# Kernel optimization log

Hardware: AMD Instinct MI355X
Metric: run time of the kernel (lower is better)

The kernel has to match this reference:

```python
import jax, jax.numpy as jnp
import numpy as np

B, S, D = 2, 2048, 2048
H, KVH, HD = 16, 4, 128
R = 128
WINDOW, GLOBAL = 512, 64
THETA = 1000000.0


def setup_inputs() -> dict:
    key = jax.random.key(0)
    ks = jax.random.split(key, 13)
    def rn(k, shape, s=0.02):
        return jax.random.normal(k, shape, dtype=jnp.float32) * s
    return {
        'x': jax.random.normal(ks[0], (B, S, D), dtype=jnp.float32),
        'wq_w': rn(ks[1], (H * HD, D)), 'wq_a': rn(ks[2], (R, D)), 'wq_b': rn(ks[3], (H * HD, R)),
        'wk_w': rn(ks[4], (KVH * HD, D)), 'wk_a': rn(ks[5], (R, D)), 'wk_b': rn(ks[6], (KVH * HD, R)),
        'wv_w': rn(ks[7], (KVH * HD, D)), 'wv_a': rn(ks[8], (R, D)), 'wv_b': rn(ks[9], (KVH * HD, R)),
        'wo_w': rn(ks[10], (D, H * HD)), 'wo_a': rn(ks[11], (R, H * HD)), 'wo_b': rn(ks[12], (D, R)),
    }


def _lora_linear(x, w, a, b):
    # F.linear(x, w) + F.linear(F.linear(x, A), B)
    return x @ w.T + (x @ a.T) @ b.T


def _apply_rope(x, cos, sin):
    # view_as_complex pairs consecutive elements: (x0,x1),(x2,x3),...
    xr, xi = x[..., 0::2], x[..., 1::2]
    out_r = xr * cos - xi * sin
    out_i = xr * sin + xi * cos
    return jnp.stack([out_r, out_i], axis=-1).reshape(x.shape)


def reference(x, wq_w, wq_a, wq_b, wk_w, wk_a, wk_b, wv_w, wv_a, wv_b, wo_w, wo_a, wo_b):
    # RoPE frequencies (scaling_factor=1.0 -> plain RoPE; YaRN ramp is identity)
    inv_freq = 1.0 / (THETA ** (jnp.arange(0, HD, 2, dtype=jnp.float32) / HD))
    t = jnp.arange(S, dtype=jnp.float32)
    freqs = t[:, None] * inv_freq[None, :]           # [S, HD/2]
    cos = jnp.cos(freqs)[None, :, None, :]           # [1,S,1,HD/2]
    sin = jnp.sin(freqs)[None, :, None, :]

    q = _lora_linear(x, wq_w, wq_a, wq_b).reshape(B, S, H, HD)
    k = _lora_linear(x, wk_w, wk_a, wk_b).reshape(B, S, KVH, HD)
    v = _lora_linear(x, wv_w, wv_a, wv_b).reshape(B, S, KVH, HD)

    q = _apply_rope(q, cos, sin)
    k = _apply_rope(k, cos, sin)

    # GQA: repeat kv heads
    g = H // KVH
    k = jnp.repeat(k, g, axis=2)
    v = jnp.repeat(v, g, axis=2)

    scores = jnp.einsum('bqhd,bkhd->bhqk', q, k) / jnp.sqrt(jnp.float32(HD))
    i = jnp.arange(S)[:, None]
    j = jnp.arange(S)[None, :]
    # causal + local sliding window + global tokens (attended by all)
    allowed = (j <= i) & (((i - j) < WINDOW) | (j < GLOBAL))
    scores = jnp.where(allowed[None, None], scores, jnp.float32(-1e9))
    p = jax.nn.softmax(scores, axis=-1)
    out = jnp.einsum('bhqk,bkhd->bqhd', p, v).reshape(B, S, H * HD)
    return _lora_linear(out, wo_w, wo_a, wo_b)
```

## Files before the change

kernel.cpp:

```cpp
#include <hip/hip_runtime.h>

#define B_ 2
#define S_LEN 2048
#define DMODEL 2048
#define NH 16
#define NKVH 4
#define HD 128
#define RLORA 128
#define WINDOW_ 512
#define NGLOBAL 64

#define FENCE asm volatile("" ::: "memory")

typedef __bf16 bf16x8 __attribute__((ext_vector_type(8)));
typedef float f32x4 __attribute__((ext_vector_type(4)));

__device__ __forceinline__ float bf2f(unsigned short h) {
    return __uint_as_float(((unsigned int)h) << 16);
}
__device__ __forceinline__ unsigned short f2bf(float f) {
    unsigned int u = __float_as_uint(f);
    unsigned int r = u + 0x7fffu + ((u >> 16) & 1u);
    return (unsigned short)(r >> 16);
}
__device__ __forceinline__ unsigned int pack2bf(float a, float b) {
    return (unsigned int)f2bf(a) | ((unsigned int)f2bf(b) << 16);
}
__device__ __forceinline__ uint4 load8f(const float* p) {
    float4 f0 = *(const float4*)p;
    float4 f1 = *(const float4*)(p + 4);
    uint4 u;
    u.x = pack2bf(f0.x, f0.y);
    u.y = pack2bf(f0.z, f0.w);
    u.z = pack2bf(f1.x, f1.y);
    u.w = pack2bf(f1.z, f1.w);
    return u;
}

__device__ __forceinline__ void gld16(const unsigned short* g, unsigned short* l) {
    __builtin_amdgcn_global_load_lds(
        (const __attribute__((address_space(1))) unsigned int*)g,
        (__attribute__((address_space(3))) unsigned int*)l,
        16, 0, 0);
}

struct Conv12 {
    const float* s[12];
    unsigned short* d[12];
    int c[13];
};
__global__ __launch_bounds__(256) void convk(Conv12 a)
{
    int b = blockIdx.x;
    int seg = 0;
    while (b >= a.c[seg + 1]) seg++;
    int off = (b - a.c[seg]) * 2048 + threadIdx.x * 8;
    *(uint4*)(a.d[seg] + off) = load8f(a.s[seg] + off);
}

struct TransA4 { const float* s[4]; unsigned short* d[4]; };
__global__ __launch_bounds__(256) void transAk(TransA4 a)
{
    __shared__ float tile[32][65];
    const int bid = blockIdx.x;
    const int mat = bid >> 7;
    const int tl = bid & 127;
    const int rt = tl & 3, ct = tl >> 2;
    const float* src = a.s[mat];
    unsigned short* dst = a.d[mat];
    const int t = threadIdx.x;
    #pragma unroll
    for (int p = 0; p < 2; p++) {
        int r = p * 16 + (t >> 4);
        int c = (t & 15) * 4;
        float4 v = *(const float4*)(src + (size_t)(rt * 32 + r) * 2048 + ct * 64 + c);
        tile[r][c] = v.x; tile[r][c + 1] = v.y;
        tile[r][c + 2] = v.z; tile[r][c + 3] = v.w;
    }
    __syncthreads();
    const int n = t >> 2, r8 = (t & 3) * 8;
    uint4 u;
    u.x = pack2bf(tile[r8 + 0][n], tile[r8 + 1][n]);
    u.y = pack2bf(tile[r8 + 2][n], tile[r8 + 3][n]);
    u.z = pack2bf(tile[r8 + 4][n], tile[r8 + 5][n]);
    u.w = pack2bf(tile[r8 + 6][n], tile[r8 + 7][n]);
    *(uint4*)(dst + (size_t)(ct * 64 + n) * 128 + rt * 32 + r8) = u;
}

__global__ __launch_bounds__(256) void weffk(
    unsigned short* __restrict__ C, int ldc,
    const unsigned short* __restrict__ Bm,
    const unsigned short* __restrict__ At,
    int seg)
{
    const int m0 = blockIdx.x * 128;
    const int n0 = blockIdx.y * 128;
    const unsigned short* Atb = At;
    if (seg)
        Atb = At + ((m0 < 2048) ? 0 : (m0 < 2560) ? (2048 * 128) : (2 * 2048 * 128));
    __shared__ __align__(16) unsigned short As_[128 * 32];
    __shared__ __align__(16) unsigned short Bs_[128 * 32];
    const int tid = threadIdx.x, lane = tid & 63, wid = tid >> 6;
    const int quad = lane >> 4, l16 = lane & 15;
    const int lr = lane >> 2, lc8 = (lane & 3) * 8;
    const int wm0 = (wid >> 1) * 64, wn0 = (wid & 1) * 64;
    f32x4 acc[4][4] = {};
    for (int k0 = 0; k0 < 128; k0 += 32) {
        #pragma unroll
        for (int c = 0; c < 2; c++) {
            int chunk = wid * 2 + c;
            gld16(Bm + (size_t)(m0 + chunk * 16 + lr) * 128 + k0 + lc8, As_ + chunk * 512);
            gld16(Atb + (size_t)(n0 + chunk * 16 + lr) * 128 + k0 + lc8, Bs_ + chunk * 512);
        }
        __syncthreads();
        bf16x8 af[4], bf[4];
        #pragma unroll
        for (int i = 0; i < 4; i++)
            af[i] = *(const bf16x8*)&As_[(wm0 + i * 16 + l16) * 32 + quad * 8];
        #pragma unroll
        for (int j = 0; j < 4; j++)
            bf[j] = *(const bf16x8*)&Bs_[(wn0 + j * 16 + l16) * 32 + quad * 8];
        #pragma unroll
        for (int i = 0; i < 4; i++)
            #pragma unroll
            for (int j = 0; j < 4; j++)
                acc[i][j] = __builtin_amdgcn_mfma_f32_16x16x32_bf16(af[i], bf[j], acc[i][j], 0, 0, 0);
        __syncthreads();
    }
    #pragma unroll
    for (int i = 0; i < 4; i++)
        #pragma unroll
        for (int j = 0; j < 4; j++) {
            const int col = n0 + wn0 + j * 16 + l16;
            #pragma unroll
            for (int r = 0; r < 4; r++) {
                size_t idx = (size_t)(m0 + wm0 + i * 16 + quad * 4 + r) * ldc + col;
                C[idx] = f2bf(bf2f(C[idx]) + acc[i][j][r]);
            }
        }
}

__device__ __forceinline__ void gemm128_acc(
    const unsigned short* __restrict__ A, int lda, int m0,
    const unsigned short* __restrict__ W, int ldw, int n0,
    int Kmain, f32x4 (&acc)[4][4])
{
    __shared__ __align__(16) unsigned short As[2][4096];
    __shared__ __align__(16) unsigned short Bs[2][4096];
    const int tid = threadIdx.x;
    const int lane = tid & 63, wid = tid >> 6;
    const int quad = lane >> 4, l16 = lane & 15;
    const int wm = (wid >> 1) * 64, wn = (wid & 1) * 64;

    int arow[2], acol[2];
    #pragma unroll
    for (int c = 0; c < 2; c++) {
        const int o = tid * 16 + c * 4096;
        arow[c] = o >> 6;
        acol[c] = (((tid & 3) * 16) ^ (((arow[c] >> 1) & 3) << 4)) >> 1;
    }

    const int nt = Kmain >> 5;

    auto stage = [&](int bb, int j) {
        const int k0 = j << 5;
        #pragma unroll
        for (int c = 0; c < 2; c++)
            gld16(A + (size_t)(m0 + arow[c]) * lda + k0 + acol[c],
                  &As[bb][tid * 8 + c * 2048]);
        #pragma unroll
        for (int c = 0; c < 2; c++)
            gld16(W + (size_t)(n0 + arow[c]) * ldw + k0 + acol[c],
                  &Bs[bb][tid * 8 + c * 2048]);
    };

    const int xoff = (((quad * 16) ^ (((l16 >> 1) & 3) << 4)) >> 1);
    const int ard = (wm + l16) * 32 + xoff;
    const int brd = (wn + l16) * 32 + xoff;

    stage(0, 0);
    stage(1, 1);

    for (int t = 0; t < nt; t++) {
        const int bb = t & 1;
        if (t < nt - 1) {
            asm volatile("s_waitcnt vmcnt(4)" ::: "memory");
        } else {
            asm volatile("s_waitcnt vmcnt(0)" ::: "memory");
        }
        __builtin_amdgcn_sched_barrier(0);
        FENCE; __builtin_amdgcn_s_barrier(); FENCE;

        bf16x8 af[4], bfn[4];
        #pragma unroll
        for (int mi = 0; mi < 4; mi++)
            af[mi] = *(const bf16x8*)&As[bb][ard + mi * 512];
        #pragma unroll
        for (int ni = 0; ni < 4; ni++)
            bfn[ni] = *(const bf16x8*)&Bs[bb][brd + ni * 512];

        __builtin_amdgcn_s_setprio(1);
        #pragma unroll
        for (int mi = 0; mi < 4; mi++)
            #pragma unroll
            for (int ni = 0; ni < 4; ni++)
                acc[mi][ni] = __builtin_amdgcn_mfma_f32_16x16x32_bf16(
                    af[mi], bfn[ni], acc[mi][ni], 0, 0, 0);
        __builtin_amdgcn_s_setprio(0);

        FENCE; __builtin_amdgcn_s_barrier(); FENCE;
        if (t + 2 < nt) stage(bb, t + 2);
    }
}

__device__ __forceinline__ f32x4 rope4(f32x4 v, int col, int rowbase)
{
    const int t2 = col & 127;
    const float invf = __expf(-(float)(t2 >> 1) * (13.815510557964274f / 64.0f));
    const bool ev = (t2 & 1) == 0;
    f32x4 o;
    #pragma unroll
    for (int r = 0; r < 4; r++) {
        float self = v[r];
        float other = __shfl_xor(self, 1);
        float pos = (float)((rowbase + r) & (S_LEN - 1));
        float s, c;
        __sincosf(pos * invf, &s, &c);
        o[r] = ev ? (self * c - other * s) : (other * s + self * c);
    }
    return o;
}

__global__ __launch_bounds__(256, 3) void gemm128_qkv(
    const unsigned short* __restrict__ Xb,
    const unsigned short* __restrict__ Wqkv,
    unsigned short* __restrict__ Qo, unsigned short* __restrict__ Ko,
    unsigned short* __restrict__ Vt)
{
    const int m0 = blockIdx.x * 128;
    const int n0 = blockIdx.y * 128;
    f32x4 acc[4][4] = {};
    gemm128_acc(Xb, DMODEL, m0, Wqkv, DMODEL, n0, DMODEL, acc);

    const int tid = threadIdx.x, lane = tid & 63, wid = tid >> 6;
    const int l16 = lane & 15, quad = lane >> 4;
    const int wm = (wid >> 1) * 64, wn = (wid & 1) * 64;

    if (n0 < 2048) {
        #pragma unroll
        for (int mi = 0; mi < 4; mi++)
            #pragma unroll
            for (int ni = 0; ni < 4; ni++) {
                const int col = n0 + wn + ni * 16 + l16;
                const int rb = m0 + wm + mi * 16 + quad * 4;
                f32x4 v = rope4(acc[mi][ni], col, rb);
                #pragma unroll
                for (int r = 0; r < 4; r++)
                    Qo[(size_t)(rb + r) * DMODEL + col] = f2bf(v[r]);
            }
    } else if (n0 < 2560) {
        #pragma unroll
        for (int mi = 0; mi < 4; mi++)
            #pragma unroll
            for (int ni = 0; ni < 4; ni++) {
                const int col = n0 - 2048 + wn + ni * 16 + l16;
                const int rb = m0 + wm + mi * 16 + quad * 4;
                f32x4 v = rope4(acc[mi][ni], col, rb);
                #pragma unroll
                for (int r = 0; r < 4; r++)
                    Ko[(size_t)(rb + r) * 512 + col] = f2bf(v[r]);
            }
    } else {
        const int b = m0 >> 11;
        #pragma unroll
        for (int mi = 0; mi < 4; mi++)
            #pragma unroll
            for (int ni = 0; ni < 4; ni++) {
                const int ncol = n0 - 2560 + wn + ni * 16 + l16;
                const int head = ncol >> 7, dd = ncol & 127;
                const int srow = (m0 & (S_LEN - 1)) + wm + mi * 16 + quad * 4;
                uint2 pk;
                pk.x = pack2bf(acc[mi][ni][0], acc[mi][ni][1]);
                pk.y = pack2bf(acc[mi][ni][2], acc[mi][ni][3]);
                *(uint2*)(Vt + ((size_t)(b * NKVH + head) * HD + dd) * S_LEN + srow) = pk;
            }
    }
}

__global__ __launch_bounds__(256, 3) void gemm128_out(
    const unsigned short* __restrict__ Xb,
    const unsigned short* __restrict__ Ww,
    float* __restrict__ Out)
{
    const int m0 = blockIdx.x * 128;
    const int n0 = blockIdx.y * 128;
    f32x4 acc[4][4] = {};
    gemm128_acc(Xb, DMODEL, m0, Ww, DMODEL, n0, DMODEL, acc);

    const int tid = threadIdx.x, lane = tid & 63, wid = tid >> 6;
    const int l16 = lane & 15, quad = lane >> 4;
    const int wm = (wid >> 1) * 64, wn = (wid & 1) * 64;
    #pragma unroll
    for (int mi = 0; mi < 4; mi++)
        #pragma unroll
        for (int ni = 0; ni < 4; ni++) {
            const int col = n0 + wn + ni * 16 + l16;
            const size_t rb = (size_t)(m0 + wm + mi * 16 + quad * 4);
            #pragma unroll
            for (int r = 0; r < 4; r++)
                Out[(rb + r) * DMODEL + col] = acc[mi][ni][r];
        }
}

__global__ __launch_bounds__(256, 2) void attn_mfma(
    const unsigned short* __restrict__ Q,
    const unsigned short* __restrict__ K,
    const unsigned short* __restrict__ Vt,
    unsigned short* __restrict__ O)
{
    __shared__ __align__(16) unsigned short kvbuf[2][8192];
    __shared__ unsigned short plds[4][32 * 40];
    const int tid = threadIdx.x, lane = tid & 63, wid = tid >> 6;
    const int l16 = lane & 15, quad = lane >> 4;
    const int bid = blockIdx.x;
    const int g   = bid & 7;
    const int kvh = g & 3;
    const int b   = g >> 2;
    const int qt  = 63 - (bid >> 3);
    const int q0  = qt * 32;
    const int h   = kvh * 4 + wid;

    const unsigned short* qrow0 = Q + ((size_t)(b * S_LEN + q0 + l16)) * DMODEL + h * HD;
    bf16x8 qf0[4], qf1[4];
    #pragma unroll
    for (int c = 0; c < 4; c++) {
        qf0[c] = *(const bf16x8*)(qrow0 + c * 32 + quad * 8);
        qf1[c] = *(const bf16x8*)(qrow0 + (size_t)16 * DMODEL + c * 32 + quad * 8);
    }

    const unsigned short* Kbase  = K + ((size_t)(b * S_LEN)) * (NKVH * HD) + kvh * HD;
    const unsigned short* Vplane = Vt + ((size_t)(b * NKVH + kvh) * HD) * S_LEN;
    unsigned short* pw = &plds[wid][0];

    const unsigned short* Ksrc[2];
    const unsigned short* Vsrc[2];
    #pragma unroll
    for (int c = 0; c < 2; c++) {
        const int o = wid * 2048 + c * 1024 + lane * 16;
        const int kkey = o >> 8;
        const int kdim = (o & 255) ^ ((kkey & 15) << 4);
        Ksrc[c] = Kbase + (size_t)kkey * (NKVH * HD) + (kdim >> 1);
        const int vd = o >> 6;
        const int vkb = (o & 63) ^ ((vd & 3) << 4);
        Vsrc[c] = Vplane + (size_t)vd * S_LEN + (vkb >> 1);
    }

    f32x4 oacc0[8] = {}, oacc1[8] = {};
    f32x4 lrow0 = {0.f, 0.f, 0.f, 0.f}, lrow1 = {0.f, 0.f, 0.f, 0.f};
    const float c2 = 0.12753102f;

    const int kthi = (q0 + 31) >> 5;
    int wlo = q0 - (WINDOW_ - 1); if (wlo < 0) wlo = 0;
    const int ktw = wlo >> 5;

    auto nexttile = [&](int t) -> int {
        if (t < ktw) { int u = t + 1; return (u < 2 && u < ktw) ? u : ktw; }
        return t + 1;
    };

    auto stage = [&](int buf, int ktb) {
        #pragma unroll
        for (int c = 0; c < 2; c++) {
            gld16(Ksrc[c] + (size_t)ktb * (NKVH * HD),
                  &kvbuf[buf][wid * 1024 + c * 512]);
            gld16(Vsrc[c] + ktb,
                  &kvbuf[buf][4096 + wid * 1024 + c * 512]);
        }
    };

    int kt = 0;
    stage(0, 0);
    __syncthreads();
    int cur = 0;

    while (true) {
        const int ktb = kt * 32;
        const int ktn = nexttile(kt);
        const bool last = (ktn > kthi);
        if (!last) stage(cur ^ 1, ktn * 32);

        const unsigned short* kb  = kvbuf[cur];
        const unsigned short* vbp = kvbuf[cur] + 4096;

        bf16x8 kf0[4], kf1[4];
        #pragma unroll
        for (int c = 0; c < 4; c++) {
            const int koff = (l16 * 256 + ((c * 64 + quad * 16) ^ (l16 << 4))) >> 1;
            kf0[c] = *(const bf16x8*)&kb[koff];
            kf1[c] = *(const bf16x8*)&kb[koff + 2048];
        }

        f32x4 s00 = {}, s01 = {}, s10 = {}, s11 = {};
        __builtin_amdgcn_s_setprio(1);
        #pragma unroll
        for (int c = 0; c < 4; c++) {
            s00 = __builtin_amdgcn_mfma_f32_16x16x32_bf16(qf0[c], kf0[c], s00, 0, 0, 0);
            s01 = __builtin_amdgcn_mfma_f32_16x16x32_bf16(qf0[c], kf1[c], s01, 0, 0, 0);
            s10 = __builtin_amdgcn_mfma_f32_16x16x32_bf16(qf1[c], kf0[c], s10, 0, 0, 0);
            s11 = __builtin_amdgcn_mfma_f32_16x16x32_bf16(qf1[c], kf1[c], s11, 0, 0, 0);
        }
        __builtin_amdgcn_s_setprio(0);

        #pragma unroll
        for (int s = 0; s < 2; s++) {
            const f32x4 sa0 = s ? s10 : s00;
            const f32x4 sa1 = s ? s11 : s01;
            const int qs = q0 + s * 16;
            const bool full = (ktb + 31 <= qs) &&
                              (((qs + 15) - ktb < WINDOW_) || (ktb + 31 < NGLOBAL));
            f32x4& lr = s ? lrow1 : lrow0;
            #pragma unroll
            for (int rr = 0; rr < 4; rr++) {
                float p0 = exp2f(sa0[rr] * c2);
                float p1 = exp2f(sa1[rr] * c2);
                if (!full) {
                    const int i = qs + quad * 4 + rr;
                    const int j0 = ktb + l16, j1 = j0 + 16;
                    bool a0 = (j0 <= i) && ((i - j0 < WINDOW_) || (j0 < NGLOBAL));
                    bool a1 = (j1 <= i) && ((i - j1 < WINDOW_) || (j1 < NGLOBAL));
                    p0 = a0 ? p0 : 0.f;
                    p1 = a1 ? p1 : 0.f;
                }
                lr[rr] += p0 + p1;
                pw[(s * 16 + quad * 4 + rr) * 40 + l16]      = f2bf(p0);
                pw[(s * 16 + quad * 4 + rr) * 40 + 16 + l16] = f2bf(p1);
            }
        }
        bf16x8 pa0 = *(const bf16x8*)(pw + l16 * 40 + quad * 8);
        bf16x8 pa1 = *(const bf16x8*)(pw + (16 + l16) * 40 + quad * 8);

        {
            bf16x8 va[4];
            #pragma unroll
            for (int ds = 0; ds < 4; ds++) {
                const int d = ds * 16 + l16;
                va[ds] = *(const bf16x8*)&vbp[(d * 64 + ((quad * 16) ^ ((l16 & 3) << 4))) >> 1];
            }
            __builtin_amdgcn_s_setprio(1);
            #pragma unroll
            for (int ds = 0; ds < 4; ds++) {
                oacc0[ds] = __builtin_amdgcn_mfma_f32_16x16x32_bf16(pa0, va[ds], oacc0[ds], 0, 0, 0);
                oacc1[ds] = __builtin_amdgcn_mfma_f32_16x16x32_bf16(pa1, va[ds], oacc1[ds], 0, 0, 0);
            }
            __builtin_amdgcn_s_setprio(0);
        }
        {
            bf16x8 vb[4];
            #pragma unroll
            for (int ds = 0; ds < 4; ds++) {
                const int d = (ds + 4) * 16 + l16;
                vb[ds] = *(const bf16x8*)&vbp[(d * 64 + ((quad * 16) ^ ((l16 & 3) << 4))) >> 1];
            }
            __builtin_amdgcn_s_setprio(1);
            #pragma unroll
            for (int ds = 0; ds < 4; ds++) {
                oacc0[ds + 4] = __builtin_amdgcn_mfma_f32_16x16x32_bf16(pa0, vb[ds], oacc0[ds + 4], 0, 0, 0);
                oacc1[ds + 4] = __builtin_amdgcn_mfma_f32_16x16x32_bf16(pa1, vb[ds], oacc1[ds + 4], 0, 0, 0);
            }
            __builtin_amdgcn_s_setprio(0);
        }

        if (last) break;
        __syncthreads();
        cur ^= 1;
        kt = ktn;
    }

    #pragma unroll
    for (int off = 1; off <= 8; off <<= 1) {
        #pragma unroll
        for (int rr = 0; rr < 4; rr++) {
            lrow0[rr] += __shfl_xor(lrow0[rr], off);
            lrow1[rr] += __shfl_xor(lrow1[rr], off);
        }
    }

    #pragma unroll
    for (int s = 0; s < 2; s++) {
        const f32x4& lr = s ? lrow1 : lrow0;
        #pragma unroll
        for (int rr = 0; rr < 4; rr++) {
            float inv = 1.f / lr[rr];
            unsigned short* orow = O + ((size_t)(b * S_LEN + q0 + s * 16 + quad * 4 + rr)) * DMODEL + h * HD;
            #pragma unroll
            for (int ds = 0; ds < 8; ds++) {
                float v = s ? oacc1[ds][rr] : oacc0[ds][rr];
                orow[ds * 16 + l16] = f2bf(v * inv);
            }
        }
    }
}

extern "C" void kernel_launch(void* const* d_in, const int* in_sizes, int n_in,
                              void* d_out, int out_size, void* d_ws, size_t ws_size,
                              hipStream_t stream)
{
    const float* x    = (const float*)d_in[0];
    const float* wq_w = (const float*)d_in[1];
    const float* wq_a = (const float*)d_in[2];
    const float* wq_b = (const float*)d_in[3];
    const float* wk_w = (const float*)d_in[4];
    const float* wk_a = (const float*)d_in[5];
    const float* wk_b = (const float*)d_in[6];
    const float* wv_w = (const float*)d_in[7];
    const float* wv_a = (const float*)d_in[8];
    const float* wv_b = (const float*)d_in[9];
    const float* wo_w = (const float*)d_in[10];
    const float* wo_a = (const float*)d_in[11];
    const float* wo_b = (const float*)d_in[12];

    char* ws = (char*)d_ws;
    unsigned short* wqkvb  = (unsigned short*)(ws);
    unsigned short* apackT = (unsigned short*)(ws + 12582912);
    unsigned short* bqkvb  = (unsigned short*)(ws + 14155776);
    unsigned short* Qbuf   = (unsigned short*)(ws + 18087936);
    unsigned short* Kbuf   = (unsigned short*)(ws + 34865152);
    unsigned short* Vtbuf  = (unsigned short*)(ws + 39059456);
    unsigned short* wowb   = (unsigned short*)(ws);
    unsigned short* wobb   = (unsigned short*)(ws + 8388608);
    unsigned short* woabT  = (unsigned short*)(ws + 8912896);
    unsigned short* xb = (unsigned short*)d_out;

    Conv12 c1;
    c1.s[0] = x;    c1.d[0] = xb;
    c1.s[1] = wq_w; c1.d[1] = wqkvb;
    c1.s[2] = wk_w; c1.d[2] = wqkvb + 2048 * 2048;
    c1.s[3] = wv_w; c1.d[3] = wqkvb + 2560 * 2048;
    c1.s[4] = wq_b; c1.d[4] = bqkvb;
    c1.s[5] = wk_b; c1.d[5] = bqkvb + 2048 * 128;
    c1.s[6] = wv_b; c1.d[6] = bqkvb + 2560 * 128;
    for (int i = 7; i < 12; i++) { c1.s[i] = wv_b; c1.d[i] = bqkvb + 2560 * 128; }
    int cum1[13] = {0, 4096, 6144, 6656, 7168, 7296, 7328, 7360, 7360, 7360,
                    7360, 7360, 7360};
    for (int i = 0; i < 13; i++) c1.c[i] = cum1[i];
    convk<<<dim3(7360), dim3(256), 0, stream>>>(c1);

    TransA4 t1;
    t1.s[0] = wq_a; t1.d[0] = apackT;
    t1.s[1] = wk_a; t1.d[1] = apackT + 2048 * 128;
    t1.s[2] = wv_a; t1.d[2] = apackT + 2 * 2048 * 128;
    t1.s[3] = wq_a; t1.d[3] = apackT;
    transAk<<<dim3(384), dim3(256), 0, stream>>>(t1);

    weffk<<<dim3(24, 16), dim3(256), 0, stream>>>(wqkvb, DMODEL, bqkvb, apackT, 1);

    gemm128_qkv<<<dim3(32, 24), dim3(256), 0, stream>>>(
        xb, wqkvb, Qbuf, Kbuf, Vtbuf);

    Conv12 c2;
    c2.s[0] = wo_w; c2.d[0] = wowb;
    c2.s[1] = wo_b; c2.d[1] = wobb;
    for (int i = 2; i < 12; i++) { c2.s[i] = wo_b; c2.d[i] = wobb; }
    int cum2[13] = {0, 2048, 2176, 2176, 2176, 2176, 2176, 2176, 2176, 2176,
                    2176, 2176, 2176};
    for (int i = 0; i < 13; i++) c2.c[i] = cum2[i];
    convk<<<dim3(2176), dim3(256), 0, stream>>>(c2);

    TransA4 t2;
    t2.s[0] = wo_a; t2.d[0] = woabT;
    t2.s[1] = wo_a; t2.d[1] = woabT;
    t2.s[2] = wo_a; t2.d[2] = woabT;
    t2.s[3] = wo_a; t2.d[3] = woabT;
    transAk<<<dim3(128), dim3(256), 0, stream>>>(t2);

    weffk<<<dim3(16, 16), dim3(256), 0, stream>>>(wowb, DMODEL, wobb, woabT, 0);

    attn_mfma<<<dim3(512), dim3(256), 0, stream>>>(Qbuf, Kbuf, Vtbuf, Qbuf);

    gemm128_out<<<dim3(32, 16), dim3(256), 0, stream>>>(
        Qbuf, wowb, (float*)d_out);
}
```

Before: 317.0 us.

## Fuse weight fp32 conversion into LoRA merge, triple-buffer GEMM, raise attention occupancy

```diff
diff --git a/kernel.cpp b/kernel.cpp
--- a/kernel.cpp
+++ b/kernel.cpp
@@ -89,6 +89,8 @@
 
 __global__ __launch_bounds__(256) void weffk(
     unsigned short* __restrict__ C, int ldc,
+    const float* __restrict__ W0, const float* __restrict__ W1,
+    const float* __restrict__ W2,
     const unsigned short* __restrict__ Bm,
     const unsigned short* __restrict__ At,
     int seg)
@@ -96,8 +98,12 @@
     const int m0 = blockIdx.x * 128;
     const int n0 = blockIdx.y * 128;
     const unsigned short* Atb = At;
-    if (seg)
-        Atb = At + ((m0 < 2048) ? 0 : (m0 < 2560) ? (2048 * 128) : (2 * 2048 * 128));
+    const float* Wsrc = W0;
+    int wrow = m0;
+    if (seg) {
+        if (m0 >= 2560)      { Atb = At + 2 * 2048 * 128; Wsrc = W2; wrow = m0 - 2560; }
+        else if (m0 >= 2048) { Atb = At + 2048 * 128;     Wsrc = W1; wrow = m0 - 2048; }
+    }
     __shared__ __align__(16) unsigned short As_[128 * 32];
     __shared__ __align__(16) unsigned short Bs_[128 * 32];
     const int tid = threadIdx.x, lane = tid & 63, wid = tid >> 6;
@@ -134,8 +140,9 @@
             const int col = n0 + wn0 + j * 16 + l16;
             #pragma unroll
             for (int r = 0; r < 4; r++) {
-                size_t idx = (size_t)(m0 + wm0 + i * 16 + quad * 4 + r) * ldc + col;
-                C[idx] = f2bf(bf2f(C[idx]) + acc[i][j][r]);
+                const int row = wm0 + i * 16 + quad * 4 + r;
+                float w = Wsrc[(size_t)(wrow + row) * 2048 + col];
+                C[(size_t)(m0 + row) * ldc + col] = f2bf(w + acc[i][j][r]);
             }
         }
 }
@@ -145,8 +152,8 @@
     const unsigned short* __restrict__ W, int ldw, int n0,
     int Kmain, f32x4 (&acc)[4][4])
 {
-    __shared__ __align__(16) unsigned short As[2][4096];
-    __shared__ __align__(16) unsigned short Bs[2][4096];
+    __shared__ __align__(16) unsigned short As[3][4096];
+    __shared__ __align__(16) unsigned short Bs[3][4096];
     const int tid = threadIdx.x;
     const int lane = tid & 63, wid = tid >> 6;
     const int quad = lane >> 4, l16 = lane & 15;
@@ -181,8 +188,8 @@
     stage(0, 0);
     stage(1, 1);
 
+    int bb = 0;
     for (int t = 0; t < nt; t++) {
-        const int bb = t & 1;
         if (t < nt - 1) {
             asm volatile("s_waitcnt vmcnt(4)" ::: "memory");
         } else {
@@ -208,8 +215,11 @@
                     af[mi], bfn[ni], acc[mi][ni], 0, 0, 0);
         __builtin_amdgcn_s_setprio(0);
 
-        FENCE; __builtin_amdgcn_s_barrier(); FENCE;
-        if (t + 2 < nt) stage(bb, t + 2);
+        if (t + 2 < nt) {
+            int sb = bb + 2; if (sb >= 3) sb -= 3;
+            stage(sb, t + 2);
+        }
+        bb = (bb == 2) ? 0 : bb + 1;
     }
 }
 
@@ -312,7 +322,7 @@
         }
 }
 
-__global__ __launch_bounds__(256, 2) void attn_mfma(
+__global__ __launch_bounds__(256, 3) void attn_mfma(
     const unsigned short* __restrict__ Q,
     const unsigned short* __restrict__ K,
     const unsigned short* __restrict__ Vt,
@@ -533,17 +543,14 @@
 
     Conv12 c1;
     c1.s[0] = x;    c1.d[0] = xb;
-    c1.s[1] = wq_w; c1.d[1] = wqkvb;
-    c1.s[2] = wk_w; c1.d[2] = wqkvb + 2048 * 2048;
-    c1.s[3] = wv_w; c1.d[3] = wqkvb + 2560 * 2048;
-    c1.s[4] = wq_b; c1.d[4] = bqkvb;
-    c1.s[5] = wk_b; c1.d[5] = bqkvb + 2048 * 128;
-    c1.s[6] = wv_b; c1.d[6] = bqkvb + 2560 * 128;
-    for (int i = 7; i < 12; i++) { c1.s[i] = wv_b; c1.d[i] = bqkvb + 2560 * 128; }
-    int cum1[13] = {0, 4096, 6144, 6656, 7168, 7296, 7328, 7360, 7360, 7360,
-                    7360, 7360, 7360};
+    c1.s[1] = wq_b; c1.d[1] = bqkvb;
+    c1.s[2] = wk_b; c1.d[2] = bqkvb + 2048 * 128;
+    c1.s[3] = wv_b; c1.d[3] = bqkvb + 2560 * 128;
+    for (int i = 4; i < 12; i++) { c1.s[i] = wv_b; c1.d[i] = bqkvb + 2560 * 128; }
+    int cum1[13] = {0, 4096, 4224, 4256, 4288, 4288, 4288, 4288, 4288, 4288,
+                    4288, 4288, 4288};
     for (int i = 0; i < 13; i++) c1.c[i] = cum1[i];
-    convk<<<dim3(7360), dim3(256), 0, stream>>>(c1);
+    convk<<<dim3(4288), dim3(256), 0, stream>>>(c1);
 
     TransA4 t1;
     t1.s[0] = wq_a; t1.d[0] = apackT;
@@ -552,19 +559,19 @@
     t1.s[3] = wq_a; t1.d[3] = apackT;
     transAk<<<dim3(384), dim3(256), 0, stream>>>(t1);
 
-    weffk<<<dim3(24, 16), dim3(256), 0, stream>>>(wqkvb, DMODEL, bqkvb, apackT, 1);
+    weffk<<<dim3(24, 16), dim3(256), 0, stream>>>(
+        wqkvb, DMODEL, wq_w, wk_w, wv_w, bqkvb, apackT, 1);
 
     gemm128_qkv<<<dim3(32, 24), dim3(256), 0, stream>>>(
         xb, wqkvb, Qbuf, Kbuf, Vtbuf);
 
     Conv12 c2;
-    c2.s[0] = wo_w; c2.d[0] = wowb;
-    c2.s[1] = wo_b; c2.d[1] = wobb;
-    for (int i = 2; i < 12; i++) { c2.s[i] = wo_b; c2.d[i] = wobb; }
-    int cum2[13] = {0, 2048, 2176, 2176, 2176, 2176, 2176, 2176, 2176, 2176,
-                    2176, 2176, 2176};
+    c2.s[0] = wo_b; c2.d[0] = wobb;
+    for (int i = 1; i < 12; i++) { c2.s[i] = wo_b; c2.d[i] = wobb; }
+    int cum2[13] = {0, 128, 128, 128, 128, 128, 128, 128, 128, 128,
+                    128, 128, 128};
     for (int i = 0; i < 13; i++) c2.c[i] = cum2[i];
-    convk<<<dim3(2176), dim3(256), 0, stream>>>(c2);
+    convk<<<dim3(128), dim3(256), 0, stream>>>(c2);
 
     TransA4 t2;
     t2.s[0] = wo_a; t2.d[0] = woabT;
@@ -573,7 +580,8 @@
     t2.s[3] = wo_a; t2.d[3] = woabT;
     transAk<<<dim3(128), dim3(256), 0, stream>>>(t2);
 
-    weffk<<<dim3(16, 16), dim3(256), 0, stream>>>(wowb, DMODEL, wobb, woabT, 0);
+    weffk<<<dim3(16, 16), dim3(256), 0, stream>>>(
+        wowb, DMODEL, wo_w, wo_w, wo_w, wobb, woabT, 0);
 
     attn_mfma<<<dim3(512), dim3(256), 0, stream>>>(Qbuf, Kbuf, Vtbuf, Qbuf);
 
```

Result: faster. 308.1 us (-2.8%).
